# Performance work log

Measured on AMD Instinct MI355X. Metric: run time of the kernel, lower is better.

Reference implementation:

```python
import jax, jax.numpy as jnp
import numpy as np

H = 16          # num_heads
D = 1024        # in_features
NH = D // H     # per-head dim
EPS = 1e-5


def _ln(x, g, b):
    m = jnp.mean(x, axis=-1, keepdims=True)
    v = jnp.mean((x - m) ** 2, axis=-1, keepdims=True)
    return (x - m) / jnp.sqrt(v + EPS) * g + b


def _mha(q, k, v, Wq, bq, Wk, bk, Wv, bv, causal):
    # q: [Tq,B,D], k/v: [Tk,B,D]
    Tq, B, _ = q.shape
    Tk = k.shape[0]
    qh = (q @ Wq + bq).reshape(Tq, B, H, NH)
    kh = (k @ Wk + bk).reshape(Tk, B, H, NH)
    vh = (v @ Wv + bv).reshape(Tk, B, H, NH)
    scale = 1.0 / np.float32(np.sqrt(NH))
    logits = jnp.einsum('qbhd,kbhd->bhqk', qh, kh) * scale  # [B,H,Tq,Tk]
    if causal:
        mask = jnp.tril(jnp.ones((Tq, Tk), dtype=bool))
        logits = jnp.where(mask, logits, -jnp.inf)  # softmax over prefix [0..t]
    w = jax.nn.softmax(logits, axis=-1)
    out = jnp.einsum('bhqk,kbhd->qbhd', w, vh).reshape(Tq, B, D)
    return out


def setup_inputs() -> dict:
    key = jax.random.key(0)
    ks = jax.random.split(key, 12)
    s = 0.02
    T, B = 1024, 8
    inp = {
        'encoder_input': jax.random.normal(ks[0], (T, B, D), jnp.float32),
        'decoder_input': jax.random.normal(ks[1], (T, B, D), jnp.float32),
        # self-attention projections
        'Wq1': jax.random.normal(ks[2], (D, D), jnp.float32) * s,
        'bq1': jnp.zeros((D,), jnp.float32),
        'Wk1': jax.random.normal(ks[3], (D, D), jnp.float32) * s,
        'bk1': jnp.zeros((D,), jnp.float32),
        'Wv1': jax.random.normal(ks[4], (D, D), jnp.float32) * s,
        'bv1': jnp.zeros((D,), jnp.float32),
        # cross-attention projections
        'Wq2': jax.random.normal(ks[5], (D, D), jnp.float32) * s,
        'bq2': jnp.zeros((D,), jnp.float32),
        'Wk2': jax.random.normal(ks[6], (D, D), jnp.float32) * s,
        'bk2': jnp.zeros((D,), jnp.float32),
        'Wv2': jax.random.normal(ks[7], (D, D), jnp.float32) * s,
        'bv2': jnp.zeros((D,), jnp.float32),
        # position-wise linear
        'Wl': jax.random.normal(ks[8], (D, D), jnp.float32) * s,
        'bl': jnp.zeros((D,), jnp.float32),
        # layernorms
        'g1': jnp.ones((D,), jnp.float32), 'be1': jnp.zeros((D,), jnp.float32),
        'g2': jnp.ones((D,), jnp.float32), 'be2': jnp.zeros((D,), jnp.float32),
        'g3': jnp.ones((D,), jnp.float32), 'be3': jnp.zeros((D,), jnp.float32),
    }
    return inp


def reference(encoder_input, decoder_input,
              Wq1, bq1, Wk1, bk1, Wv1, bv1,
              Wq2, bq2, Wk2, bk2, Wv2, bv2,
              Wl, bl, g1, be1, g2, be2, g3, be3):
    # causal self-attention (prefix [:t+1] per step == causal mask)
    x = _mha(decoder_input, decoder_input, decoder_input,
             Wq1, bq1, Wk1, bk1, Wv1, bv1, causal=True)
    x = _ln(x + decoder_input, g1, be1)
    # cross-attention over full encoder input
    y = _mha(x, encoder_input, encoder_input,
             Wq2, bq2, Wk2, bk2, Wv2, bv2, causal=False)
    y = _ln(y + x, g2, be2)
    # position-wise linear (no activation in source) + residual + LN
    z = y @ Wl + bl
    out = _ln(z + y, g3, be3)
    return out
```

## Files before the change

### kernel.cpp

```cpp
#include <hip/hip_runtime.h>
#include <hip/hip_bf16.h>

typedef __bf16 bf16x8 __attribute__((ext_vector_type(8)));
typedef float f32x4 __attribute__((ext_vector_type(4)));

#define MFMA16(A, B, C) __builtin_amdgcn_mfma_f32_16x16x32_bf16(A, B, C, 0, 0, 0)

#define GLDS(gp, lp)                                                              \
    __builtin_amdgcn_global_load_lds(                                             \
        (const __attribute__((address_space(1))) void*)(gp),                      \
        (__attribute__((address_space(3))) void*)(lp), 16, 0, 0)

__global__ __launch_bounds__(256) void wt_transpose(const float* __restrict__ W,
                                                    __hip_bfloat16* __restrict__ Wt,
                                                    int K, int N) {
    __shared__ float tile[32][33];
    const int bn = blockIdx.x * 32;
    const int bk = blockIdx.y * 32;
    const int tx = threadIdx.x, ty = threadIdx.y;
#pragma unroll
    for (int i = 0; i < 4; i++) {
        tile[ty + i * 8][tx] = W[(size_t)(bk + ty + i * 8) * N + bn + tx];
    }
    __syncthreads();
#pragma unroll
    for (int i = 0; i < 4; i++) {
        Wt[(size_t)(bn + ty + i * 8) * K + bk + tx] = __float2bfloat16(tile[tx][ty + i * 8]);
    }
}

__global__ __launch_bounds__(256) void to_bf16(const float* __restrict__ x,
                                               __hip_bfloat16* __restrict__ y, int n) {
    const int i = (blockIdx.x * 256 + threadIdx.x) * 4;
    if (i >= n) return;
    const float4 v = *(const float4*)(x + i);
    __align__(8) __hip_bfloat16 t[4] = {__float2bfloat16(v.x), __float2bfloat16(v.y),
                                        __float2bfloat16(v.z), __float2bfloat16(v.w)};
    *(uint2*)(y + i) = *(const uint2*)t;
}

__global__ __launch_bounds__(256) void gemm_bias_kernel(
    const __hip_bfloat16* __restrict__ A, const __hip_bfloat16* __restrict__ Bt,
    const float* __restrict__ bias, float* __restrict__ Cf,
    __hip_bfloat16* __restrict__ Cb, int M, int N, int K) {
    __shared__ __align__(16) __hip_bfloat16 As[128 * 32];
    __shared__ __align__(16) __hip_bfloat16 Bs[128 * 32];
    const int tid = threadIdx.x;
    const int wave = tid >> 6, lane = tid & 63;
    const int quad = lane >> 4, l16 = lane & 15;
    const int m0 = blockIdx.x * 128, n0 = blockIdx.y * 128;
    const int wm = (wave & 1) * 64, wn = (wave >> 1) * 64;
    const int srow = wave * 16 + (lane >> 2);
    const int scol = (lane & 3) * 8;
    const __hip_bfloat16* Ap0 = A + (size_t)(m0 + srow) * K + scol;
    const __hip_bfloat16* Ap1 = A + (size_t)(m0 + 64 + srow) * K + scol;
    const __hip_bfloat16* Bp0 = Bt + (size_t)(n0 + srow) * K + scol;
    const __hip_bfloat16* Bp1 = Bt + (size_t)(n0 + 64 + srow) * K + scol;
    __hip_bfloat16* Al0 = &As[wave * 512];
    __hip_bfloat16* Al1 = &As[2048 + wave * 512];
    __hip_bfloat16* Bl0 = &Bs[wave * 512];
    __hip_bfloat16* Bl1 = &Bs[2048 + wave * 512];
    f32x4 acc[4][4] = {};
    for (int k0 = 0; k0 < K; k0 += 32) {
        GLDS(Ap0 + k0, Al0);
        GLDS(Ap1 + k0, Al1);
        GLDS(Bp0 + k0, Bl0);
        GLDS(Bp1 + k0, Bl1);
        __syncthreads();
        bf16x8 af[4], bfr[4];
#pragma unroll
        for (int i = 0; i < 4; i++) {
            af[i] = *(const bf16x8*)(&As[(wm + i * 16 + l16) * 32 + quad * 8]);
            bfr[i] = *(const bf16x8*)(&Bs[(wn + i * 16 + l16) * 32 + quad * 8]);
        }
        __syncthreads();
#pragma unroll
        for (int i = 0; i < 4; i++)
#pragma unroll
            for (int j = 0; j < 4; j++)
                acc[i][j] = MFMA16(af[i], bfr[j], acc[i][j]);
    }
#pragma unroll
    for (int i = 0; i < 4; i++) {
#pragma unroll
        for (int j = 0; j < 4; j++) {
            const int mr = m0 + wm + i * 16 + quad * 4;
            const int nc = n0 + wn + j * 16 + l16;
            const float bv = bias[nc];
#pragma unroll
            for (int r = 0; r < 4; r++) {
                const float v = acc[i][j][r] + bv;
                const size_t idx = (size_t)(mr + r) * N + nc;
                if (Cf) Cf[idx] = v;
                if (Cb) Cb[idx] = __float2bfloat16(v);
            }
        }
    }
}

__global__ __launch_bounds__(256) void attn_kernel(
    const __hip_bfloat16* __restrict__ Qp, const __hip_bfloat16* __restrict__ Kp,
    const __hip_bfloat16* __restrict__ Vp, float* __restrict__ Op,
    int T, int Bb, int qRS, int kvRS, int causal) {
    constexpr int LDK = 72, LDV = 72, LDP = 72;
    __shared__ __align__(16) __hip_bfloat16 Ks[64 * LDK];
    __shared__ __align__(16) __hip_bfloat16 Vs[64 * LDV];
    __shared__ __align__(16) __hip_bfloat16 Ps[4][16 * LDP];
    const int tid = threadIdx.x, wave = tid >> 6, lane = tid & 63;
    const int quad = lane >> 4, l16 = lane & 15;
    const int bh = blockIdx.y;
    const int b = bh % Bb;
    const int h = bh / Bb;
    const int q0 = blockIdx.x * 64;
    const size_t qbase = (size_t)b * qRS + h * 64;
    const size_t kbase = (size_t)b * kvRS + h * 64;
    const int qstride = Bb * qRS, kstride = Bb * kvRS;
    const size_t obase = (size_t)b * 1024 + h * 64;
    const int ostride = Bb * 1024;
    const float SC = 0.125f;

    const int myq = q0 + wave * 16 + l16;
    bf16x8 qf0, qf1;
    {
        const __hip_bfloat16* qptr = Qp + qbase + (size_t)myq * qstride;
        qf0 = *(const bf16x8*)(qptr + quad * 8);
        qf1 = *(const bf16x8*)(qptr + 32 + quad * 8);
    }
    float m_i = -1e30f, l_i = 0.f;
    f32x4 o[4] = {};

    const int kend = causal ? (q0 + 64) : T;
    for (int k0 = 0; k0 < kend; k0 += 64) {
        __syncthreads();
        {
            const int key = tid >> 2, dd = (tid & 3) * 16;
            const __hip_bfloat16* kp2 = Kp + kbase + (size_t)(k0 + key) * kstride + dd;
            *(uint4*)(&Ks[key * LDK + dd]) = *(const uint4*)(kp2);
            *(uint4*)(&Ks[key * LDK + dd + 8]) = *(const uint4*)(kp2 + 8);
            const __hip_bfloat16* vp2 = Vp + kbase + (size_t)(k0 + key) * kstride + dd;
            __align__(16) __hip_bfloat16 tmp[16];
            *(uint4*)(tmp) = *(const uint4*)(vp2);
            *(uint4*)(tmp + 8) = *(const uint4*)(vp2 + 8);
            const int kb = key >> 3, k7 = key & 7;
#pragma unroll
            for (int j = 0; j < 16; j++) {
                const int d = dd + j;
                const int blk = kb ^ ((d >> 4) << 1);
                Vs[d * LDV + blk * 8 + k7] = tmp[j];
            }
        }
        __syncthreads();
        f32x4 s[4];
#pragma unroll
        for (int n = 0; n < 4; n++) {
            f32x4 z = {};
            const bf16x8 kf0 = *(const bf16x8*)(&Ks[(n * 16 + l16) * LDK + quad * 8]);
            const bf16x8 kf1 = *(const bf16x8*)(&Ks[(n * 16 + l16) * LDK + 32 + quad * 8]);
            z = MFMA16(kf0, qf0, z);
            z = MFMA16(kf1, qf1, z);
            s[n] = z;
        }
        const bool nm = causal && (k0 + 63 > q0 + wave * 16);
        float mx = -1e30f;
#pragma unroll
        for (int n = 0; n < 4; n++) {
#pragma unroll
            for (int r = 0; r < 4; r++) {
                float sv = s[n][r] * SC;
                if (nm && (k0 + n * 16 + quad * 4 + r > myq)) sv = -1e30f;
                s[n][r] = sv;
                mx = fmaxf(mx, sv);
            }
        }
        mx = fmaxf(mx, __shfl_xor(mx, 16));
        mx = fmaxf(mx, __shfl_xor(mx, 32));
        const float mnew = fmaxf(m_i, mx);
        const float alpha = __expf(m_i - mnew);
        m_i = mnew;
        float sum = 0.f;
#pragma unroll
        for (int n = 0; n < 4; n++) {
            __align__(8) __hip_bfloat16 pb[4];
#pragma unroll
            for (int r = 0; r < 4; r++) {
                const float pv = __expf(s[n][r] - m_i);
                sum += pv;
                pb[r] = __float2bfloat16(pv);
            }
            *(uint2*)(&Ps[wave][l16 * LDP + n * 16 + quad * 4]) = *(const uint2*)pb;
        }
        sum += __shfl_xor(sum, 16);
        sum += __shfl_xor(sum, 32);
        l_i = l_i * alpha + sum;
#pragma unroll
        for (int mm = 0; mm < 4; mm++)
#pragma unroll
            for (int r = 0; r < 4; r++) o[mm][r] *= alpha;
        __syncthreads();
        const bf16x8 pf0 = *(const bf16x8*)(&Ps[wave][l16 * LDP + quad * 8]);
        const bf16x8 pf1 = *(const bf16x8*)(&Ps[wave][l16 * LDP + 32 + quad * 8]);
#pragma unroll
        for (int mm = 0; mm < 4; mm++) {
            const int blk0 = quad ^ (mm << 1);
            const int blk1 = (4 + quad) ^ (mm << 1);
            const bf16x8 vf0 = *(const bf16x8*)(&Vs[(mm * 16 + l16) * LDV + blk0 * 8]);
            const bf16x8 vf1 = *(const bf16x8*)(&Vs[(mm * 16 + l16) * LDV + blk1 * 8]);
            o[mm] = MFMA16(vf0, pf0, o[mm]);
            o[mm] = MFMA16(vf1, pf1, o[mm]);
        }
    }
    const float inv = 1.0f / l_i;
    float* ob = Op + obase + (size_t)myq * ostride;
#pragma unroll
    for (int mm = 0; mm < 4; mm++) {
        float4 vv = make_float4(o[mm][0] * inv, o[mm][1] * inv, o[mm][2] * inv,
                                o[mm][3] * inv);
        *(float4*)(ob + mm * 16 + quad * 4) = vv;
    }
}

__global__ __launch_bounds__(256) void ln_res_kernel(
    const float* __restrict__ a, const float* __restrict__ bres,
    const float* __restrict__ g, const float* __restrict__ be,
    float* __restrict__ outf, __hip_bfloat16* __restrict__ outb) {
    const int row = blockIdx.x;
    const int tid = threadIdx.x;
    const size_t off = (size_t)row * 1024 + tid * 4;
    const float4 va = *(const float4*)(a + off);
    const float4 vb = *(const float4*)(bres + off);
    float x0 = va.x + vb.x, x1 = va.y + vb.y, x2 = va.z + vb.z, x3 = va.w + vb.w;
    float s = x0 + x1 + x2 + x3;
    float ss = x0 * x0 + x1 * x1 + x2 * x2 + x3 * x3;
#pragma unroll
    for (int w = 32; w >= 1; w >>= 1) {
        s += __shfl_xor(s, w);
        ss += __shfl_xor(ss, w);
    }
    __shared__ float sm[4], sv[4];
    const int wave = tid >> 6;
    if ((tid & 63) == 0) { sm[wave] = s; sv[wave] = ss; }
    __syncthreads();
    s = sm[0] + sm[1] + sm[2] + sm[3];
    ss = sv[0] + sv[1] + sv[2] + sv[3];
    const float mean = s * (1.f / 1024.f);
    const float inv = rsqrtf(ss * (1.f / 1024.f) - mean * mean + 1e-5f);
    const float4 gg = *(const float4*)(g + tid * 4);
    const float4 bb = *(const float4*)(be + tid * 4);
    const float y0 = (x0 - mean) * inv * gg.x + bb.x;
    const float y1 = (x1 - mean) * inv * gg.y + bb.y;
    const float y2 = (x2 - mean) * inv * gg.z + bb.z;
    const float y3 = (x3 - mean) * inv * gg.w + bb.w;
    *(float4*)(outf + off) = make_float4(y0, y1, y2, y3);
    if (outb) {
        __align__(8) __hip_bfloat16 t[4] = {__float2bfloat16(y0), __float2bfloat16(y1),
                                            __float2bfloat16(y2), __float2bfloat16(y3)};
        *(uint2*)(outb + off) = *(const uint2*)t;
    }
}

extern "C" void kernel_launch(void* const* d_in, const int* in_sizes, int n_in,
                              void* d_out, int out_size, void* d_ws, size_t ws_size,
                              hipStream_t stream) {
    const float* enc = (const float*)d_in[0];
    const float* dec = (const float*)d_in[1];
    const float* Wq1 = (const float*)d_in[2];
    const float* bq1 = (const float*)d_in[3];
    const float* Wk1 = (const float*)d_in[4];
    const float* bk1 = (const float*)d_in[5];
    const float* Wv1 = (const float*)d_in[6];
    const float* bv1 = (const float*)d_in[7];
    const float* Wq2 = (const float*)d_in[8];
    const float* bq2 = (const float*)d_in[9];
    const float* Wk2 = (const float*)d_in[10];
    const float* bk2 = (const float*)d_in[11];
    const float* Wv2 = (const float*)d_in[12];
    const float* bv2 = (const float*)d_in[13];
    const float* Wl = (const float*)d_in[14];
    const float* bl = (const float*)d_in[15];
    const float* g1 = (const float*)d_in[16];
    const float* be1 = (const float*)d_in[17];
    const float* g2 = (const float*)d_in[18];
    const float* be2 = (const float*)d_in[19];
    const float* g3 = (const float*)d_in[20];
    const float* be3 = (const float*)d_in[21];
    float* outp = (float*)d_out;

    char* p = (char*)d_ws;
    auto alloc = [&](size_t n) {
        char* r = p;
        p += (n + 255) & ~(size_t)255;
        return r;
    };
    const size_t MD = (size_t)8192 * 1024;
    __hip_bfloat16* enc_b = (__hip_bfloat16*)alloc(MD * 2);
    __hip_bfloat16* dec_b = (__hip_bfloat16*)alloc(MD * 2);
    __hip_bfloat16* Wt = (__hip_bfloat16*)alloc((size_t)7 * 1024 * 1024 * 2);
    float* bcat = (float*)alloc((3072 + 2048) * sizeof(float));
    __hip_bfloat16* qkv = (__hip_bfloat16*)alloc(MD * 3 * 2);
    __hip_bfloat16* qb = (__hip_bfloat16*)alloc(MD * 2);
    float* attnf = (float*)alloc(MD * 4);
    float* xf = (float*)alloc(MD * 4);
    float* yf = (float*)alloc(MD * 4);
    __hip_bfloat16* xb = dec_b;
    __hip_bfloat16* yb = enc_b;

    const float* Ws[7] = {Wq1, Wk1, Wv1, Wq2, Wk2, Wv2, Wl};
    for (int i = 0; i < 7; i++) {
        wt_transpose<<<dim3(32, 32), dim3(32, 8), 0, stream>>>(
            Ws[i], Wt + (size_t)i * 1024 * 1024, 1024, 1024);
    }
    to_bf16<<<8192, 256, 0, stream>>>(enc, enc_b, (int)MD);
    to_bf16<<<8192, 256, 0, stream>>>(dec, dec_b, (int)MD);
    hipMemcpyAsync(bcat, bq1, 4096, hipMemcpyDeviceToDevice, stream);
    hipMemcpyAsync(bcat + 1024, bk1, 4096, hipMemcpyDeviceToDevice, stream);
    hipMemcpyAsync(bcat + 2048, bv1, 4096, hipMemcpyDeviceToDevice, stream);
    hipMemcpyAsync(bcat + 3072, bk2, 4096, hipMemcpyDeviceToDevice, stream);
    hipMemcpyAsync(bcat + 4096, bv2, 4096, hipMemcpyDeviceToDevice, stream);

    gemm_bias_kernel<<<dim3(64, 24), 256, 0, stream>>>(dec_b, Wt, bcat, nullptr, qkv,
                                                       8192, 3072, 1024);
    attn_kernel<<<dim3(16, 128), 256, 0, stream>>>(qkv, qkv + 1024, qkv + 2048, attnf,
                                                   1024, 8, 3072, 3072, 1);
    ln_res_kernel<<<8192, 256, 0, stream>>>(attnf, dec, g1, be1, xf, xb);

    gemm_bias_kernel<<<dim3(64, 8), 256, 0, stream>>>(
        xb, Wt + (size_t)3 * 1024 * 1024, bq2, nullptr, qb, 8192, 1024, 1024);
    gemm_bias_kernel<<<dim3(64, 16), 256, 0, stream>>>(
        enc_b, Wt + (size_t)4 * 1024 * 1024, bcat + 3072, nullptr, qkv, 8192, 2048, 1024);
    attn_kernel<<<dim3(16, 128), 256, 0, stream>>>(qb, qkv, qkv + 1024, attnf,
                                                   1024, 8, 1024, 2048, 0);
    ln_res_kernel<<<8192, 256, 0, stream>>>(attnf, xf, g2, be2, yf, yb);

    gemm_bias_kernel<<<dim3(64, 8), 256, 0, stream>>>(
        yb, Wt + (size_t)6 * 1024 * 1024, bl, attnf, nullptr, 8192, 1024, 1024);
    ln_res_kernel<<<8192, 256, 0, stream>>>(attnf, yf, g3, be3, outp, nullptr);
}
```

Baseline: 602.1 us.

## Batch prep launches, deepen GEMM K-tile, pre-transpose V, emit bf16 intermediates

Merges the seven weight transposes, the two fp32-to-bf16 conversions and the bias memcpys into single batched launches. The GEMM K tile grows from 32 to 64 with XOR-swizzled LDS. A separate kernel now pre-transposes V so attention can load K and V tiles with direct global-to-LDS loads instead of per-element scattered LDS stores. Attention uses exp2 with a folded log2e scale, drops one barrier, and writes bf16 output; the final linear layer's output is also stored in bf16, halving intermediate traffic at some precision cost.

```diff
diff --git a/kernel.cpp b/kernel.cpp
--- a/kernel.cpp
+++ b/kernel.cpp
@@ -11,74 +11,118 @@
         (const __attribute__((address_space(1))) void*)(gp),                      \
         (__attribute__((address_space(3))) void*)(lp), 16, 0, 0)
 
-__global__ __launch_bounds__(256) void wt_transpose(const float* __restrict__ W,
-                                                    __hip_bfloat16* __restrict__ Wt,
-                                                    int K, int N) {
+struct PtrW { const float* p[7]; };
+__global__ __launch_bounds__(256) void wt_transpose(PtrW W, __hip_bfloat16* __restrict__ Wt) {
+    const float* __restrict__ src = W.p[blockIdx.z];
+    __hip_bfloat16* __restrict__ dst = Wt + ((size_t)blockIdx.z << 20);
     __shared__ float tile[32][33];
     const int bn = blockIdx.x * 32;
     const int bk = blockIdx.y * 32;
     const int tx = threadIdx.x, ty = threadIdx.y;
 #pragma unroll
     for (int i = 0; i < 4; i++) {
-        tile[ty + i * 8][tx] = W[(size_t)(bk + ty + i * 8) * N + bn + tx];
+        tile[ty + i * 8][tx] = src[(size_t)(bk + ty + i * 8) * 1024 + bn + tx];
     }
     __syncthreads();
 #pragma unroll
     for (int i = 0; i < 4; i++) {
-        Wt[(size_t)(bn + ty + i * 8) * K + bk + tx] = __float2bfloat16(tile[tx][ty + i * 8]);
-    }
-}
-
-__global__ __launch_bounds__(256) void to_bf16(const float* __restrict__ x,
-                                               __hip_bfloat16* __restrict__ y, int n) {
+        dst[(size_t)(bn + ty + i * 8) * 1024 + bk + tx] =
+            __float2bfloat16(tile[tx][ty + i * 8]);
+    }
+}
+
+struct PtrC { const float* s[2]; __hip_bfloat16* d[2]; };
+__global__ __launch_bounds__(256) void to_bf16(PtrC c) {
+    const int z = blockIdx.y;
     const int i = (blockIdx.x * 256 + threadIdx.x) * 4;
-    if (i >= n) return;
-    const float4 v = *(const float4*)(x + i);
+    const float4 v = *(const float4*)(c.s[z] + i);
     __align__(8) __hip_bfloat16 t[4] = {__float2bfloat16(v.x), __float2bfloat16(v.y),
                                         __float2bfloat16(v.z), __float2bfloat16(v.w)};
-    *(uint2*)(y + i) = *(const uint2*)t;
+    *(uint2*)(c.d[z] + i) = *(const uint2*)t;
+}
+
+struct Ptr5 { const float* p[5]; };
+__global__ __launch_bounds__(256) void bias_concat(Ptr5 srcs, float* __restrict__ dst) {
+    const int i = threadIdx.x * 4;
+    *(float4*)(dst + blockIdx.x * 1024 + i) = *(const float4*)(srcs.p[blockIdx.x] + i);
+}
+
+__global__ __launch_bounds__(256) void v_transpose(const __hip_bfloat16* __restrict__ src,
+                                                   __hip_bfloat16* __restrict__ Vt,
+                                                   int S, int coloff) {
+    __shared__ __hip_bfloat16 tile[64][72];
+    const int t0 = blockIdx.x * 64;
+    const int bh = blockIdx.y;
+    const int b = bh & 7, h = bh >> 3;
+    const int tid = threadIdx.x;
+    const int r = tid >> 2, c = (tid & 3) * 16;
+    const __hip_bfloat16* sp =
+        src + (size_t)((t0 + r) * 8 + b) * S + coloff + h * 64 + c;
+    *(uint4*)(&tile[r][c]) = *(const uint4*)(sp);
+    *(uint4*)(&tile[r][c + 8]) = *(const uint4*)(sp + 8);
+    __syncthreads();
+    const int d = tid >> 2, tc = (tid & 3) * 16;
+    __align__(16) __hip_bfloat16 tmp[16];
+#pragma unroll
+    for (int j = 0; j < 16; j++) tmp[j] = tile[tc + j][d];
+    __hip_bfloat16* op = Vt + ((size_t)(b * 16 + h) << 16) + (size_t)d * 1024 + t0 + tc;
+    *(uint4*)(op) = *(const uint4*)(tmp);
+    *(uint4*)(op + 8) = *(const uint4*)(tmp + 8);
 }
 
 __global__ __launch_bounds__(256) void gemm_bias_kernel(
     const __hip_bfloat16* __restrict__ A, const __hip_bfloat16* __restrict__ Bt,
     const float* __restrict__ bias, float* __restrict__ Cf,
     __hip_bfloat16* __restrict__ Cb, int M, int N, int K) {
-    __shared__ __align__(16) __hip_bfloat16 As[128 * 32];
-    __shared__ __align__(16) __hip_bfloat16 Bs[128 * 32];
+    __shared__ __align__(16) __hip_bfloat16 As[128 * 64];
+    __shared__ __align__(16) __hip_bfloat16 Bs[128 * 64];
     const int tid = threadIdx.x;
     const int wave = tid >> 6, lane = tid & 63;
     const int quad = lane >> 4, l16 = lane & 15;
     const int m0 = blockIdx.x * 128, n0 = blockIdx.y * 128;
     const int wm = (wave & 1) * 64, wn = (wave >> 1) * 64;
-    const int srow = wave * 16 + (lane >> 2);
-    const int scol = (lane & 3) * 8;
-    const __hip_bfloat16* Ap0 = A + (size_t)(m0 + srow) * K + scol;
-    const __hip_bfloat16* Ap1 = A + (size_t)(m0 + 64 + srow) * K + scol;
-    const __hip_bfloat16* Bp0 = Bt + (size_t)(n0 + srow) * K + scol;
-    const __hip_bfloat16* Bp1 = Bt + (size_t)(n0 + 64 + srow) * K + scol;
-    __hip_bfloat16* Al0 = &As[wave * 512];
-    __hip_bfloat16* Al1 = &As[2048 + wave * 512];
-    __hip_bfloat16* Bl0 = &Bs[wave * 512];
-    __hip_bfloat16* Bl1 = &Bs[2048 + wave * 512];
+    const int lrow = lane >> 3;
+    const int lch = (lane & 7) ^ (lrow & 7);
+    const int sw = l16 & 7;
+    const __hip_bfloat16* ap[4];
+    const __hip_bfloat16* bp[4];
+    __hip_bfloat16* al[4];
+    __hip_bfloat16* bl[4];
+#pragma unroll
+    for (int u = 0; u < 4; u++) {
+        const int q = wave * 4 + u;
+        const int row = q * 8 + lrow;
+        ap[u] = A + (size_t)(m0 + row) * K + lch * 8;
+        bp[u] = Bt + (size_t)(n0 + row) * K + lch * 8;
+        al[u] = &As[q * 512];
+        bl[u] = &Bs[q * 512];
+    }
     f32x4 acc[4][4] = {};
-    for (int k0 = 0; k0 < K; k0 += 32) {
-        GLDS(Ap0 + k0, Al0);
-        GLDS(Ap1 + k0, Al1);
-        GLDS(Bp0 + k0, Bl0);
-        GLDS(Bp1 + k0, Bl1);
+    for (int k0 = 0; k0 < K; k0 += 64) {
+#pragma unroll
+        for (int u = 0; u < 4; u++) {
+            GLDS(ap[u] + k0, al[u]);
+            GLDS(bp[u] + k0, bl[u]);
+        }
         __syncthreads();
-        bf16x8 af[4], bfr[4];
-#pragma unroll
-        for (int i = 0; i < 4; i++) {
-            af[i] = *(const bf16x8*)(&As[(wm + i * 16 + l16) * 32 + quad * 8]);
-            bfr[i] = *(const bf16x8*)(&Bs[(wn + i * 16 + l16) * 32 + quad * 8]);
-        }
+        bf16x8 af[2][4], bfr[2][4];
+#pragma unroll
+        for (int h2 = 0; h2 < 2; h2++)
+#pragma unroll
+            for (int i = 0; i < 4; i++) {
+                af[h2][i] = *(const bf16x8*)(&As[(wm + i * 16 + l16) * 64 +
+                                                 (((h2 * 4 + quad) ^ sw) << 3)]);
+                bfr[h2][i] = *(const bf16x8*)(&Bs[(wn + i * 16 + l16) * 64 +
+                                                  (((h2 * 4 + quad) ^ sw) << 3)]);
+            }
         __syncthreads();
 #pragma unroll
-        for (int i = 0; i < 4; i++)
-#pragma unroll
-            for (int j = 0; j < 4; j++)
-                acc[i][j] = MFMA16(af[i], bfr[j], acc[i][j]);
+        for (int h2 = 0; h2 < 2; h2++)
+#pragma unroll
+            for (int i = 0; i < 4; i++)
+#pragma unroll
+                for (int j = 0; j < 4; j++)
+                    acc[i][j] = MFMA16(af[h2][i], bfr[h2][j], acc[i][j]);
     }
 #pragma unroll
     for (int i = 0; i < 4; i++) {
@@ -100,62 +144,57 @@
 
 __global__ __launch_bounds__(256) void attn_kernel(
     const __hip_bfloat16* __restrict__ Qp, const __hip_bfloat16* __restrict__ Kp,
-    const __hip_bfloat16* __restrict__ Vp, float* __restrict__ Op,
-    int T, int Bb, int qRS, int kvRS, int causal) {
-    constexpr int LDK = 72, LDV = 72, LDP = 72;
-    __shared__ __align__(16) __hip_bfloat16 Ks[64 * LDK];
-    __shared__ __align__(16) __hip_bfloat16 Vs[64 * LDV];
-    __shared__ __align__(16) __hip_bfloat16 Ps[4][16 * LDP];
+    const __hip_bfloat16* __restrict__ Vt, __hip_bfloat16* __restrict__ Ob,
+    int T, int qRS, int kRS, int causal) {
+    __shared__ __align__(16) __hip_bfloat16 Ks[64 * 64];
+    __shared__ __align__(16) __hip_bfloat16 Vs[64 * 64];
+    __shared__ __align__(16) __hip_bfloat16 Ps[4][16 * 64];
     const int tid = threadIdx.x, wave = tid >> 6, lane = tid & 63;
     const int quad = lane >> 4, l16 = lane & 15;
-    const int bh = blockIdx.y;
-    const int b = bh % Bb;
-    const int h = bh / Bb;
+    const int bh = blockIdx.y, b = bh & 7, h = bh >> 3;
     const int q0 = blockIdx.x * 64;
-    const size_t qbase = (size_t)b * qRS + h * 64;
-    const size_t kbase = (size_t)b * kvRS + h * 64;
-    const int qstride = Bb * qRS, kstride = Bb * kvRS;
-    const size_t obase = (size_t)b * 1024 + h * 64;
-    const int ostride = Bb * 1024;
-    const float SC = 0.125f;
+    const int qstride = 8 * qRS, kstride = 8 * kRS;
+    const int sw = l16 & 7;
+    const float SCL = 0.18033688f;
 
     const int myq = q0 + wave * 16 + l16;
     bf16x8 qf0, qf1;
     {
-        const __hip_bfloat16* qptr = Qp + qbase + (size_t)myq * qstride;
+        const __hip_bfloat16* qptr = Qp + (size_t)b * qRS + h * 64 + (size_t)myq * qstride;
         qf0 = *(const bf16x8*)(qptr + quad * 8);
         qf1 = *(const bf16x8*)(qptr + 32 + quad * 8);
     }
+    const int jk = wave * 2;
+    const int lrow = lane >> 3;
+    const int lch = (lane & 7) ^ (lrow & 7);
+    const __hip_bfloat16* kp0 =
+        Kp + (size_t)b * kRS + h * 64 + (size_t)(jk * 8 + lrow) * kstride + lch * 8;
+    const __hip_bfloat16* kp1 = kp0 + (size_t)8 * kstride;
+    const __hip_bfloat16* vp0 =
+        Vt + ((size_t)(b * 16 + h) << 16) + (size_t)(jk * 8 + lrow) * 1024 + lch * 8;
+    const __hip_bfloat16* vp1 = vp0 + 8 * 1024;
+    __hip_bfloat16* kl0 = &Ks[jk * 512];
+    __hip_bfloat16* kl1 = &Ks[jk * 512 + 512];
+    __hip_bfloat16* vl0 = &Vs[jk * 512];
+    __hip_bfloat16* vl1 = &Vs[jk * 512 + 512];
+
     float m_i = -1e30f, l_i = 0.f;
     f32x4 o[4] = {};
-
     const int kend = causal ? (q0 + 64) : T;
     for (int k0 = 0; k0 < kend; k0 += 64) {
         __syncthreads();
-        {
-            const int key = tid >> 2, dd = (tid & 3) * 16;
-            const __hip_bfloat16* kp2 = Kp + kbase + (size_t)(k0 + key) * kstride + dd;
-            *(uint4*)(&Ks[key * LDK + dd]) = *(const uint4*)(kp2);
-            *(uint4*)(&Ks[key * LDK + dd + 8]) = *(const uint4*)(kp2 + 8);
-            const __hip_bfloat16* vp2 = Vp + kbase + (size_t)(k0 + key) * kstride + dd;
-            __align__(16) __hip_bfloat16 tmp[16];
-            *(uint4*)(tmp) = *(const uint4*)(vp2);
-            *(uint4*)(tmp + 8) = *(const uint4*)(vp2 + 8);
-            const int kb = key >> 3, k7 = key & 7;
-#pragma unroll
-            for (int j = 0; j < 16; j++) {
-                const int d = dd + j;
-                const int blk = kb ^ ((d >> 4) << 1);
-                Vs[d * LDV + blk * 8 + k7] = tmp[j];
-            }
-        }
+        GLDS(kp0 + (size_t)k0 * kstride, kl0);
+        GLDS(kp1 + (size_t)k0 * kstride, kl1);
+        GLDS(vp0 + k0, vl0);
+        GLDS(vp1 + k0, vl1);
         __syncthreads();
         f32x4 s[4];
 #pragma unroll
         for (int n = 0; n < 4; n++) {
             f32x4 z = {};
-            const bf16x8 kf0 = *(const bf16x8*)(&Ks[(n * 16 + l16) * LDK + quad * 8]);
-            const bf16x8 kf1 = *(const bf16x8*)(&Ks[(n * 16 + l16) * LDK + 32 + quad * 8]);
+            const int row = (n * 16 + l16) * 64;
+            const bf16x8 kf0 = *(const bf16x8*)(&Ks[row + ((quad ^ sw) << 3)]);
+            const bf16x8 kf1 = *(const bf16x8*)(&Ks[row + (((quad + 4) ^ sw) << 3)]);
             z = MFMA16(kf0, qf0, z);
             z = MFMA16(kf1, qf1, z);
             s[n] = z;
@@ -166,7 +205,7 @@
         for (int n = 0; n < 4; n++) {
 #pragma unroll
             for (int r = 0; r < 4; r++) {
-                float sv = s[n][r] * SC;
+                float sv = s[n][r] * SCL;
                 if (nm && (k0 + n * 16 + quad * 4 + r > myq)) sv = -1e30f;
                 s[n][r] = sv;
                 mx = fmaxf(mx, sv);
@@ -175,7 +214,7 @@
         mx = fmaxf(mx, __shfl_xor(mx, 16));
         mx = fmaxf(mx, __shfl_xor(mx, 32));
         const float mnew = fmaxf(m_i, mx);
-        const float alpha = __expf(m_i - mnew);
+        const float alpha = exp2f(m_i - mnew);
         m_i = mnew;
         float sum = 0.f;
 #pragma unroll
@@ -183,52 +222,56 @@
             __align__(8) __hip_bfloat16 pb[4];
 #pragma unroll
             for (int r = 0; r < 4; r++) {
-                const float pv = __expf(s[n][r] - m_i);
+                const float pv = exp2f(s[n][r] - m_i);
                 sum += pv;
                 pb[r] = __float2bfloat16(pv);
             }
-            *(uint2*)(&Ps[wave][l16 * LDP + n * 16 + quad * 4]) = *(const uint2*)pb;
+            const int gcp = 2 * n + (quad >> 1);
+            *(uint2*)(&Ps[wave][l16 * 64 + ((gcp ^ sw) << 3) + (quad & 1) * 4]) =
+                *(const uint2*)pb;
         }
         sum += __shfl_xor(sum, 16);
         sum += __shfl_xor(sum, 32);
         l_i = l_i * alpha + sum;
 #pragma unroll
-        for (int mm = 0; mm < 4; mm++)
-#pragma unroll
-            for (int r = 0; r < 4; r++) o[mm][r] *= alpha;
-        __syncthreads();
-        const bf16x8 pf0 = *(const bf16x8*)(&Ps[wave][l16 * LDP + quad * 8]);
-        const bf16x8 pf1 = *(const bf16x8*)(&Ps[wave][l16 * LDP + 32 + quad * 8]);
+        for (int mm = 0; mm < 4; mm++) o[mm] = o[mm] * alpha;
+        const bf16x8 pf0 = *(const bf16x8*)(&Ps[wave][l16 * 64 + ((quad ^ sw) << 3)]);
+        const bf16x8 pf1 =
+            *(const bf16x8*)(&Ps[wave][l16 * 64 + (((quad + 4) ^ sw) << 3)]);
 #pragma unroll
         for (int mm = 0; mm < 4; mm++) {
-            const int blk0 = quad ^ (mm << 1);
-            const int blk1 = (4 + quad) ^ (mm << 1);
-            const bf16x8 vf0 = *(const bf16x8*)(&Vs[(mm * 16 + l16) * LDV + blk0 * 8]);
-            const bf16x8 vf1 = *(const bf16x8*)(&Vs[(mm * 16 + l16) * LDV + blk1 * 8]);
+            const int vrow = (mm * 16 + l16) * 64;
+            const bf16x8 vf0 = *(const bf16x8*)(&Vs[vrow + ((quad ^ sw) << 3)]);
+            const bf16x8 vf1 = *(const bf16x8*)(&Vs[vrow + (((quad + 4) ^ sw) << 3)]);
             o[mm] = MFMA16(vf0, pf0, o[mm]);
             o[mm] = MFMA16(vf1, pf1, o[mm]);
         }
     }
     const float inv = 1.0f / l_i;
-    float* ob = Op + obase + (size_t)myq * ostride;
+    __hip_bfloat16* ob = Ob + (size_t)b * 1024 + h * 64 + (size_t)myq * 8192;
 #pragma unroll
     for (int mm = 0; mm < 4; mm++) {
-        float4 vv = make_float4(o[mm][0] * inv, o[mm][1] * inv, o[mm][2] * inv,
-                                o[mm][3] * inv);
-        *(float4*)(ob + mm * 16 + quad * 4) = vv;
+        __align__(8) __hip_bfloat16 t[4] = {
+            __float2bfloat16(o[mm][0] * inv), __float2bfloat16(o[mm][1] * inv),
+            __float2bfloat16(o[mm][2] * inv), __float2bfloat16(o[mm][3] * inv)};
+        *(uint2*)(ob + mm * 16 + quad * 4) = *(const uint2*)t;
     }
 }
 
 __global__ __launch_bounds__(256) void ln_res_kernel(
-    const float* __restrict__ a, const float* __restrict__ bres,
+    const __hip_bfloat16* __restrict__ a, const float* __restrict__ bres,
     const float* __restrict__ g, const float* __restrict__ be,
     float* __restrict__ outf, __hip_bfloat16* __restrict__ outb) {
     const int row = blockIdx.x;
     const int tid = threadIdx.x;
     const size_t off = (size_t)row * 1024 + tid * 4;
-    const float4 va = *(const float4*)(a + off);
+    uint2 ar = *(const uint2*)(a + off);
+    const __hip_bfloat16* ah = (const __hip_bfloat16*)&ar;
     const float4 vb = *(const float4*)(bres + off);
-    float x0 = va.x + vb.x, x1 = va.y + vb.y, x2 = va.z + vb.z, x3 = va.w + vb.w;
+    float x0 = __bfloat162float(ah[0]) + vb.x;
+    float x1 = __bfloat162float(ah[1]) + vb.y;
+    float x2 = __bfloat162float(ah[2]) + vb.z;
+    float x3 = __bfloat162float(ah[3]) + vb.w;
     float s = x0 + x1 + x2 + x3;
     float ss = x0 * x0 + x1 * x1 + x2 * x2 + x3 * x3;
 #pragma unroll
@@ -250,7 +293,7 @@
     const float y1 = (x1 - mean) * inv * gg.y + bb.y;
     const float y2 = (x2 - mean) * inv * gg.z + bb.z;
     const float y3 = (x3 - mean) * inv * gg.w + bb.w;
-    *(float4*)(outf + off) = make_float4(y0, y1, y2, y3);
+    if (outf) *(float4*)(outf + off) = make_float4(y0, y1, y2, y3);
     if (outb) {
         __align__(8) __hip_bfloat16 t[4] = {__float2bfloat16(y0), __float2bfloat16(y1),
                                             __float2bfloat16(y2), __float2bfloat16(y3)};
@@ -298,40 +341,37 @@
     float* bcat = (float*)alloc((3072 + 2048) * sizeof(float));
     __hip_bfloat16* qkv = (__hip_bfloat16*)alloc(MD * 3 * 2);
     __hip_bfloat16* qb = (__hip_bfloat16*)alloc(MD * 2);
-    float* attnf = (float*)alloc(MD * 4);
+    __hip_bfloat16* attnb = (__hip_bfloat16*)alloc(MD * 2);
+    __hip_bfloat16* Vtb = (__hip_bfloat16*)alloc(MD * 2);
     float* xf = (float*)alloc(MD * 4);
     float* yf = (float*)alloc(MD * 4);
     __hip_bfloat16* xb = dec_b;
     __hip_bfloat16* yb = enc_b;
 
-    const float* Ws[7] = {Wq1, Wk1, Wv1, Wq2, Wk2, Wv2, Wl};
-    for (int i = 0; i < 7; i++) {
-        wt_transpose<<<dim3(32, 32), dim3(32, 8), 0, stream>>>(
-            Ws[i], Wt + (size_t)i * 1024 * 1024, 1024, 1024);
-    }
-    to_bf16<<<8192, 256, 0, stream>>>(enc, enc_b, (int)MD);
-    to_bf16<<<8192, 256, 0, stream>>>(dec, dec_b, (int)MD);
-    hipMemcpyAsync(bcat, bq1, 4096, hipMemcpyDeviceToDevice, stream);
-    hipMemcpyAsync(bcat + 1024, bk1, 4096, hipMemcpyDeviceToDevice, stream);
-    hipMemcpyAsync(bcat + 2048, bv1, 4096, hipMemcpyDeviceToDevice, stream);
-    hipMemcpyAsync(bcat + 3072, bk2, 4096, hipMemcpyDeviceToDevice, stream);
-    hipMemcpyAsync(bcat + 4096, bv2, 4096, hipMemcpyDeviceToDevice, stream);
+    PtrW wptrs = {{Wq1, Wk1, Wv1, Wq2, Wk2, Wv2, Wl}};
+    wt_transpose<<<dim3(32, 32, 7), dim3(32, 8), 0, stream>>>(wptrs, Wt);
+    PtrC cp = {{enc, dec}, {enc_b, dec_b}};
+    to_bf16<<<dim3(8192, 2), 256, 0, stream>>>(cp);
+    Ptr5 bp = {{bq1, bk1, bv1, bk2, bv2}};
+    bias_concat<<<5, 256, 0, stream>>>(bp, bcat);
 
     gemm_bias_kernel<<<dim3(64, 24), 256, 0, stream>>>(dec_b, Wt, bcat, nullptr, qkv,
                                                        8192, 3072, 1024);
-    attn_kernel<<<dim3(16, 128), 256, 0, stream>>>(qkv, qkv + 1024, qkv + 2048, attnf,
-                                                   1024, 8, 3072, 3072, 1);
-    ln_res_kernel<<<8192, 256, 0, stream>>>(attnf, dec, g1, be1, xf, xb);
+    v_transpose<<<dim3(16, 128), 256, 0, stream>>>(qkv, Vtb, 3072, 2048);
+    attn_kernel<<<dim3(16, 128), 256, 0, stream>>>(qkv, qkv + 1024, Vtb, attnb,
+                                                   1024, 3072, 3072, 1);
+    ln_res_kernel<<<8192, 256, 0, stream>>>(attnb, dec, g1, be1, xf, xb);
 
     gemm_bias_kernel<<<dim3(64, 8), 256, 0, stream>>>(
         xb, Wt + (size_t)3 * 1024 * 1024, bq2, nullptr, qb, 8192, 1024, 1024);
     gemm_bias_kernel<<<dim3(64, 16), 256, 0, stream>>>(
         enc_b, Wt + (size_t)4 * 1024 * 1024, bcat + 3072, nullptr, qkv, 8192, 2048, 1024);
-    attn_kernel<<<dim3(16, 128), 256, 0, stream>>>(qb, qkv, qkv + 1024, attnf,
-                                                   1024, 8, 1024, 2048, 0);
-    ln_res_kernel<<<8192, 256, 0, stream>>>(attnf, xf, g2, be2, yf, yb);
+    v_transpose<<<dim3(16, 128), 256, 0, stream>>>(qkv, Vtb, 2048, 1024);
+    attn_kernel<<<dim3(16, 128), 256, 0, stream>>>(qb, qkv, Vtb, attnb,
+                                                   1024, 1024, 2048, 0);
+    ln_res_kernel<<<8192, 256, 0, stream>>>(attnb, xf, g2, be2, yf, yb);
 
     gemm_bias_kernel<<<dim3(64, 8), 256, 0, stream>>>(
-        yb, Wt + (size_t)6 * 1024 * 1024, bl, attnf, nullptr, 8192, 1024, 1024);
-    ln_res_kernel<<<8192, 256, 0, stream>>>(attnf, yf, g3, be3, outp, nullptr);
-}
+        yb, Wt + (size_t)6 * 1024 * 1024, bl, nullptr, qb, 8192, 1024, 1024);
+    ln_res_kernel<<<8192, 256, 0, stream>>>(qb, yf, g3, be3, outp, nullptr);
+}
```

After: 576.7 us. 1.04x faster.
